# Kernel optimization log

Measured on AMD Instinct MI355X. Metric: run time of the kernel, lower is better.

Reference implementation:

```python
import jax, jax.numpy as jnp
import numpy as np


def setup_inputs() -> dict:
    key = jax.random.key(0)
    k1, k2, k3 = jax.random.split(key, 3)
    B, C, H, W = 2, 32, 128, 256
    maxdisp = 12
    feat_l = jax.random.normal(k1, (B, C, H, W), dtype=jnp.float32)
    feat_r = jax.random.normal(k2, (B, C, H, W), dtype=jnp.float32)
    # disparity estimate in pixels at this feature scale
    disp = jax.random.uniform(k3, (B, 1, H, W), dtype=jnp.float32) * 64.0
    return {"feat_l": feat_l, "feat_r": feat_r, "disp": disp, "maxdisp": maxdisp}


def _warp_1d(feat_r, d_map):
    """Warp feat_r [B,C,H,W] horizontally by d_map [B,H,W].

    Equivalent to torch grid_sample(bilinear, zeros padding, align_corners=True)
    with grid x = xx - d, y = yy: y lands exactly on pixel centers, so the
    bilinear interp degenerates to 1-D interp along W with zero padding.
    """
    B, C, H, W = feat_r.shape
    xx = jnp.arange(W, dtype=feat_r.dtype)
    px = xx[None, None, :] - d_map  # [B,H,W] sampling x-coordinate
    x0 = jnp.floor(px)
    w1 = px - x0                     # weight of right neighbor
    w0 = 1.0 - w1
    x0i = x0.astype(jnp.int32)
    x1i = x0i + 1
    m0 = ((x0i >= 0) & (x0i <= W - 1)).astype(feat_r.dtype)  # zeros padding
    m1 = ((x1i >= 0) & (x1i <= W - 1)).astype(feat_r.dtype)

    def gather(idx):
        idxc = jnp.clip(idx, 0, W - 1)[:, None, :, :]  # [B,1,H,W]
        return jnp.take_along_axis(feat_r, jnp.broadcast_to(idxc, (B, C, H, W)), axis=3)

    g0 = gather(x0i)
    g1 = gather(x1i)
    return g0 * (w0 * m0)[:, None] + g1 * (w1 * m1)[:, None]  # [B,C,H,W]


def reference(feat_l, feat_r, disp, maxdisp):
    B, C, H, W = feat_l.shape
    D = 2 * maxdisp - 1
    shifts = jnp.arange(-maxdisp + 1, maxdisp, dtype=feat_l.dtype)  # [D]
    # batch_disp - batch_shift, laid out [D,B,H,W] (plane-major for vmap)
    d_all = disp[:, 0][None, :, :, :] - shifts[:, None, None, None]  # [D,B,H,W]
    warped = jax.vmap(lambda d: _warp_1d(feat_r, d))(d_all)          # [D,B,C,H,W]
    # L1 norm over channels of (feat_l - warped)
    cost = jnp.sum(jnp.abs(feat_l[None] - warped), axis=2)           # [D,B,H,W]
    return jnp.transpose(cost, (1, 0, 2, 3))                         # [B,D,H,W]
```

## Files before the change

### kernel.cpp

```cpp
#include <hip/hip_runtime.h>

#define BB 2
#define CC 32
#define HH 128
#define WW 256
#define DD 23
#define HW (HH * WW)

#define SEG 64
#define NSEG 4
#define NCOLS 151
#define SC 36
#define RED 23


__global__ __launch_bounds__(256, 4) void cost_volume_kernel(
    const float* __restrict__ feat_l,
    const float* __restrict__ feat_r,
    const float* __restrict__ disp,
    float* __restrict__ out)
{
    __shared__ __align__(16) float smem[NCOLS * SC];

    const int t  = threadIdx.x;
    const int q  = t >> 6;
    const int px = t & 63;
    const int s  = blockIdx.x >> 8;
    const int bh = blockIdx.x & 255;
    const int b  = bh >> 7;
    const int h  = bh & 127;
    const int w  = s * SEG + px;
    const int COL0 = s * SEG - 75;
    const int c0 = q * 8;

    float fl[8];
    const size_t lbase = ((size_t)(b * CC + c0)) * HW + (size_t)h * WW + w;
    #pragma unroll
    for (int k = 0; k < 8; ++k) fl[k] = feat_l[lbase + (size_t)k * HW];
    const float d = disp[(size_t)bh * WW + w];

    #pragma unroll
    for (int cc = 0; cc < 3; ++cc) {
        const int col = cc * 64 + px;
        if (col < NCOLS) {
            const int  gcol = col + COL0;
            const bool inr  = (gcol >= 0) && (gcol < WW);
            const int  gc   = min(max(gcol, 0), WW - 1);
            #pragma unroll
            for (int qq = 0; qq < 2; ++qq) {
                const int cq = (q + 4 * qq) * 4;
                const size_t base = ((size_t)(b * CC + cq)) * HW + (size_t)h * WW + gc;
                const float x0 = feat_r[base];
                const float x1 = feat_r[base + HW];
                const float x2 = feat_r[base + 2 * HW];
                const float x3 = feat_r[base + 3 * HW];
                float4 v;
                v.x = inr ? x0 : 0.0f;
                v.y = inr ? x1 : 0.0f;
                v.z = inr ? x2 : 0.0f;
                v.w = inr ? x3 : 0.0f;
                *(float4*)&smem[col * SC + cq] = v;
            }
        }
    }
    __syncthreads();

    const float pxf = (float)w - d;
    const float x0f = floorf(pxf);
    const float w1  = pxf - x0f;
    const float w0  = 1.0f - w1;
    int lb = (int)x0f - COL0 - 11;
    lb = min(max(lb, 0), NCOLS - 24);

    float4 Ta[3], Tb[3];
    #define LOADTAP(idx, j) { \
        const float4* p_ = (const float4*)&smem[(lb + (j)) * SC + c0]; \
        Ta[idx] = p_[0]; Tb[idx] = p_[1]; }

    LOADTAP(0, 0)
    LOADTAP(1, 1)

    float acc[DD];
    #pragma unroll
    for (int di = 0; di < DD; ++di) {
        if (di + 2 < 24) LOADTAP((di + 2) % 3, di + 2)
        const float4 A0 = Ta[di % 3],       A1 = Tb[di % 3];
        const float4 B0 = Ta[(di + 1) % 3], B1 = Tb[(di + 1) % 3];
        float sA = 0.0f, sB = 0.0f;
        sA += fabsf(fmaf(w0, A0.x, fmaf(w1, B0.x, -fl[0])));
        sB += fabsf(fmaf(w0, A0.y, fmaf(w1, B0.y, -fl[1])));
        sA += fabsf(fmaf(w0, A0.z, fmaf(w1, B0.z, -fl[2])));
        sB += fabsf(fmaf(w0, A0.w, fmaf(w1, B0.w, -fl[3])));
        sA += fabsf(fmaf(w0, A1.x, fmaf(w1, B1.x, -fl[4])));
        sB += fabsf(fmaf(w0, A1.y, fmaf(w1, B1.y, -fl[5])));
        sA += fabsf(fmaf(w0, A1.z, fmaf(w1, B1.z, -fl[6])));
        sB += fabsf(fmaf(w0, A1.w, fmaf(w1, B1.w, -fl[7])));
        acc[di] = sA + sB;
    }
    #undef LOADTAP

    __syncthreads();
    if (q != 0) {
        float* r = &smem[(q - 1) * (64 * RED) + px * RED];
        #pragma unroll
        for (int di = 0; di < DD; ++di) r[di] = acc[di];
    }
    __syncthreads();
    if (q == 0) {
        const float* r0 = &smem[0 * (64 * RED) + px * RED];
        const float* r1 = &smem[1 * (64 * RED) + px * RED];
        const float* r2 = &smem[2 * (64 * RED) + px * RED];
        #pragma unroll
        for (int di = 0; di < DD; ++di) {
            const float v = acc[di] + r0[di] + r1[di] + r2[di];
            out[((size_t)(b * DD + di)) * HW + (size_t)h * WW + w] = v;
        }
    }
}

extern "C" void kernel_launch(void* const* d_in, const int* in_sizes, int n_in,
                              void* d_out, int out_size, void* d_ws, size_t ws_size,
                              hipStream_t stream)
{
    const float* feat_l = (const float*)d_in[0];
    const float* feat_r = (const float*)d_in[1];
    const float* disp   = (const float*)d_in[2];
    float* out = (float*)d_out;

    dim3 grid(NSEG * BB * HH);
    dim3 block(256);
    cost_volume_kernel<<<grid, block, 0, stream>>>(feat_l, feat_r, disp, out);
}
```

Measured before the change: 77.83 us.

## Halve pixel segment and split channels across eight groups per block

Each block now covers 32 pixels with eight 4-channel groups instead of 64 pixels with four 8-channel groups, which doubles the grid and raises the launch-bounds occupancy target to 8 blocks. The cross-channel reduction first combines the two half-wave groups with a lane shuffle, then sums four shared-memory partials, and all threads cooperate on the final output stores. The aim is more parallelism, fewer registers per thread, and spreading the reduction and writeback across the whole block. In exchange, the relative halo overhead grows (119 staged columns for 32 pixels instead of 151 for 64), so more feat_r data is loaded per output.

```diff
diff --git a/kernel.cpp b/kernel.cpp
--- a/kernel.cpp
+++ b/kernel.cpp
@@ -7,48 +7,52 @@
 #define DD 23
 #define HW (HH * WW)
 
-#define SEG 64
-#define NSEG 4
-#define NCOLS 151
+#define SEG 32
+#define NSEG 8
+#define NCOLS 119
 #define SC 36
 #define RED 23
+#define REGION (32 * RED)
+#define SMEMF (NCOLS * SC)
 
 
-__global__ __launch_bounds__(256, 4) void cost_volume_kernel(
+__global__ __launch_bounds__(256, 8) void cost_volume_kernel(
     const float* __restrict__ feat_l,
     const float* __restrict__ feat_r,
     const float* __restrict__ disp,
     float* __restrict__ out)
 {
-    __shared__ __align__(16) float smem[NCOLS * SC];
+    __shared__ __align__(16) float smem[SMEMF];
 
-    const int t  = threadIdx.x;
-    const int q  = t >> 6;
-    const int px = t & 63;
+    const int t    = threadIdx.x;
+    const int lane = t & 63;
+    const int px   = t & 31;
+    const int cg   = t >> 5;
+    const int wv   = t >> 6;
     const int s  = blockIdx.x >> 8;
     const int bh = blockIdx.x & 255;
     const int b  = bh >> 7;
     const int h  = bh & 127;
     const int w  = s * SEG + px;
     const int COL0 = s * SEG - 75;
-    const int c0 = q * 8;
+    const int c0 = cg * 4;
 
-    float fl[8];
+    float fl[4];
     const size_t lbase = ((size_t)(b * CC + c0)) * HW + (size_t)h * WW + w;
     #pragma unroll
-    for (int k = 0; k < 8; ++k) fl[k] = feat_l[lbase + (size_t)k * HW];
+    for (int k = 0; k < 4; ++k) fl[k] = feat_l[lbase + (size_t)k * HW];
     const float d = disp[(size_t)bh * WW + w];
 
-    #pragma unroll
-    for (int cc = 0; cc < 3; ++cc) {
-        const int col = cc * 64 + px;
+    {
+        const int col = t & 127;
+        const int hq  = t >> 7;
         if (col < NCOLS) {
             const int  gcol = col + COL0;
             const bool inr  = (gcol >= 0) && (gcol < WW);
             const int  gc   = min(max(gcol, 0), WW - 1);
             #pragma unroll
-            for (int qq = 0; qq < 2; ++qq) {
-                const int cq = (q + 4 * qq) * 4;
+            for (int qq = 0; qq < 4; ++qq) {
+                const int cq = (hq * 4 + qq) * 4;
                 const size_t base = ((size_t)(b * CC + cq)) * HW + (size_t)h * WW + gc;
                 const float x0 = feat_r[base];
                 const float x1 = feat_r[base + HW];
@@ -72,10 +76,8 @@
     int lb = (int)x0f - COL0 - 11;
     lb = min(max(lb, 0), NCOLS - 24);
 
-    float4 Ta[3], Tb[3];
-    #define LOADTAP(idx, j) { \
-        const float4* p_ = (const float4*)&smem[(lb + (j)) * SC + c0]; \
-        Ta[idx] = p_[0]; Tb[idx] = p_[1]; }
+    float4 Ta[3];
+    #define LOADTAP(idx, j) Ta[idx] = *(const float4*)&smem[(lb + (j)) * SC + c0];
 
     LOADTAP(0, 0)
     LOADTAP(1, 1)
@@ -84,36 +86,36 @@
     #pragma unroll
     for (int di = 0; di < DD; ++di) {
         if (di + 2 < 24) LOADTAP((di + 2) % 3, di + 2)
-        const float4 A0 = Ta[di % 3],       A1 = Tb[di % 3];
-        const float4 B0 = Ta[(di + 1) % 3], B1 = Tb[(di + 1) % 3];
-        float sA = 0.0f, sB = 0.0f;
-        sA += fabsf(fmaf(w0, A0.x, fmaf(w1, B0.x, -fl[0])));
-        sB += fabsf(fmaf(w0, A0.y, fmaf(w1, B0.y, -fl[1])));
-        sA += fabsf(fmaf(w0, A0.z, fmaf(w1, B0.z, -fl[2])));
-        sB += fabsf(fmaf(w0, A0.w, fmaf(w1, B0.w, -fl[3])));
-        sA += fabsf(fmaf(w0, A1.x, fmaf(w1, B1.x, -fl[4])));
-        sB += fabsf(fmaf(w0, A1.y, fmaf(w1, B1.y, -fl[5])));
-        sA += fabsf(fmaf(w0, A1.z, fmaf(w1, B1.z, -fl[6])));
-        sB += fabsf(fmaf(w0, A1.w, fmaf(w1, B1.w, -fl[7])));
-        acc[di] = sA + sB;
+        const float4 A = Ta[di % 3];
+        const float4 B = Ta[(di + 1) % 3];
+        const float s0 = fabsf(fmaf(w0, A.x, fmaf(w1, B.x, -fl[0])));
+        const float s1 = fabsf(fmaf(w0, A.y, fmaf(w1, B.y, -fl[1])));
+        const float s2 = fabsf(fmaf(w0, A.z, fmaf(w1, B.z, -fl[2])));
+        const float s3 = fabsf(fmaf(w0, A.w, fmaf(w1, B.w, -fl[3])));
+        acc[di] = (s0 + s1) + (s2 + s3);
     }
     #undef LOADTAP
 
+    #pragma unroll
+    for (int di = 0; di < DD; ++di)
+        acc[di] += __shfl_xor(acc[di], 32, 64);
+
     __syncthreads();
-    if (q != 0) {
-        float* r = &smem[(q - 1) * (64 * RED) + px * RED];
+    if (lane < 32) {
+        float* r = &smem[wv * REGION + px * RED];
         #pragma unroll
         for (int di = 0; di < DD; ++di) r[di] = acc[di];
     }
     __syncthreads();
-    if (q == 0) {
-        const float* r0 = &smem[0 * (64 * RED) + px * RED];
-        const float* r1 = &smem[1 * (64 * RED) + px * RED];
-        const float* r2 = &smem[2 * (64 * RED) + px * RED];
-        #pragma unroll
-        for (int di = 0; di < DD; ++di) {
-            const float v = acc[di] + r0[di] + r1[di] + r2[di];
-            out[((size_t)(b * DD + di)) * HW + (size_t)h * WW + w] = v;
+    #pragma unroll
+    for (int k = 0; k < 3; ++k) {
+        const int o = t + 256 * k;
+        if (o < 32 * DD) {
+            const int di2 = o >> 5;
+            const int p2  = o & 31;
+            const float* r0 = &smem[p2 * RED + di2];
+            const float v = (r0[0] + r0[REGION]) + (r0[2 * REGION] + r0[3 * REGION]);
+            out[((size_t)(b * DD + di2)) * HW + (size_t)h * WW + (s * SEG + p2)] = v;
         }
     }
 }
```

Result: no change. 79.20 us (+1.8%).
